# Kernel tuning notes

Measured on AMD Instinct MI355X. Metric: run time of the kernel, lower is better.

The kernel has to match this reference:

```python
import jax, jax.numpy as jnp
import numpy as np

B, E, H, S, V, K = 128, 512, 512, 2048, 83, 3
PAD = 82


def _pos_emb(n, e):
    pos = jnp.arange(n, dtype=jnp.float32)[:, None]                      # [n,1]
    k = jnp.exp(-jnp.log(10000.0) * jnp.arange(0, e, 2, dtype=jnp.float32) / e)  # [e/2]
    arg = pos * k                                                        # [n,e/2]
    pe = jnp.stack([jnp.sin(arg), jnp.cos(arg)], axis=-1).reshape(n, e)  # interleave sin/cos
    return pe.T                                                          # [e,n]


def setup_inputs() -> dict:
    key = jax.random.key(0)
    ks = jax.random.split(key, 8)
    return {
        "encoder_output": jax.random.normal(ks[0], (B, H, S), dtype=jnp.float32),
        "encoder_total": jax.random.normal(ks[1], (B, H, S), dtype=jnp.float32),
        "decoder_input": jax.random.randint(ks[2], (B,), 0, V),
        "count": 0,
        "emb": jax.random.normal(ks[3], (V, E), dtype=jnp.float32) * 0.02,
        "conv_w": jax.random.normal(ks[4], (2 * H, E, K), dtype=jnp.float32) * 0.02,
        "conv_b": jnp.zeros((2 * H,), dtype=jnp.float32),
        "lin2_w": jax.random.normal(ks[5], (V, H), dtype=jnp.float32) * 0.02,
        "lin2_b": jnp.zeros((V,), dtype=jnp.float32),
    }


def reference(encoder_output, encoder_total, decoder_input, count, emb, conv_w, conv_b, lin2_w, lin2_b):
    # count==0 first-step path; dropout is identity (inference).
    pe3 = _pos_emb(K, E)                                    # [E,K]

    def layer(dec_in):
        # dec_in: [B,E,K]
        xp = dec_in + pe3[None]                             # positional embedding add
        y = jnp.einsum('bek,oek->bo', xp, conv_w) + conv_b  # valid conv1d, out length 1 -> [B,2H]
        a, b = jnp.split(y, 2, axis=1)
        glu = a * jax.nn.sigmoid(b)                         # [B,H]
        d = glu + xp[:, :, -1]                              # residual with last (pe-added) column
        scores = jnp.einsum('bh,bhs->bs', d, encoder_output)
        attn = jax.nn.softmax(scores, axis=-1)              # [B,S]
        c = jnp.einsum('bs,bhs->bh', attn, encoder_total)   # [B,H]
        h = glu + c
        logits = h @ lin2_w.T + lin2_b                      # [B,V]
        return h, jax.nn.log_softmax(logits, axis=-1)

    x = emb[decoder_input][:, :, None]                      # [B,E,1]
    pad_col = jnp.broadcast_to(emb[PAD][None, :, None], (B, E, 1))
    dec1 = jnp.concatenate([pad_col, pad_col, x], axis=2)   # [B,E,3]

    h1, _ = layer(dec1)                                     # n_l = 0
    dec2 = jnp.concatenate([dec1[:, :, :2], h1[:, :, None]], axis=2)
    h2, _ = layer(dec2)                                     # n_l = 1
    dec3 = jnp.concatenate([dec1[:, :, :2], h2[:, :, None]], axis=2)
    h3, ls3 = layer(dec3)                                   # n_l = 2

    return (jax.nn.softmax(h3, axis=1)[:, :, None],         # [B,H,1]
            ls3[:, None, :])                                # [B,1,V]
```

## Files before the change

kernel.cpp:

```cpp
#include <hip/hip_runtime.h>
#include <math.h>

#define B_   128
#define E_   512
#define H_   512
#define S_   2048
#define V_   83
#define PAD_ 82

typedef float v4f __attribute__((ext_vector_type(4)));

__device__ __forceinline__ v4f ldnt4(const float* p) {
    return __builtin_nontemporal_load((const v4f*)p);
}


__global__ void k_misc(const float* __restrict__ emb, float* __restrict__ pe2,
                       float* __restrict__ x01i) {
    int e = threadIdx.x;
    float freq = expf(-9.210340371976184f * (float)(e & ~1) * (1.0f / 512.0f));
    float p0 = (e & 1) ? 1.0f : 0.0f;
    float p1 = (e & 1) ? cosf(freq) : sinf(freq);
    float p2 = (e & 1) ? cosf(2.0f * freq) : sinf(2.0f * freq);
    pe2[e] = p2;
    float ep = emb[PAD_ * 512 + e];
    x01i[e * 3 + 0] = ep + p0;
    x01i[e * 3 + 1] = ep + p1;
    x01i[e * 3 + 2] = 0.0f;
}

__global__ void k_base3(const float* __restrict__ cw, const float* __restrict__ x01i,
                        float* __restrict__ base) {
    int t = threadIdx.x, w = t >> 6, lane = t & 63;
    __shared__ float xs[1536];
    for (int j = t; j < 1536; j += 256) xs[j] = x01i[j];
    __syncthreads();
    int o = blockIdx.x * 4 + w;
    const float* rp = cw + (size_t)o * 1536 + lane * 4;
    float acc = 0.f;
    #pragma unroll
    for (int j = 0; j < 6; ++j) {
        float4 v = *(const float4*)(rp + j * 256);
        const float* xp = &xs[lane * 4 + j * 256];
        acc += v.x * xp[0] + v.y * xp[1] + v.z * xp[2] + v.w * xp[3];
    }
    #pragma unroll
    for (int off = 32; off > 0; off >>= 1) acc += __shfl_down(acc, off, 64);
    if (lane == 0) base[o] = acc;
}

__global__ void k_prep(const float* __restrict__ cw, float* __restrict__ W2t) {
    __shared__ float tile[64][129];
    int ob = blockIdx.x * 64, eb = blockIdx.y * 128;
    int t = threadIdx.x;
    for (int idx = t; idx < 8192; idx += 256) {
        int r = idx >> 7, e = idx & 127;
        tile[r][e] = cw[(size_t)(ob + r) * 1536 + (eb + e) * 3 + 2];
    }
    __syncthreads();
    for (int idx = t; idx < 8192; idx += 256) {
        int e = idx >> 6, o = idx & 63;
        W2t[(size_t)(eb + e) * 1024 + ob + o] = tile[o][e];
    }
}


__global__ void k_yx(int first, const int* __restrict__ tok, const float* __restrict__ emb,
                     const float* __restrict__ h, const float* __restrict__ pe2,
                     const float* __restrict__ W2t, const float* __restrict__ base,
                     const float* __restrict__ cb, float* __restrict__ xcol,
                     float* __restrict__ y) {
    int oc = blockIdx.x, bq = blockIdx.y, t = threadIdx.x;
    __shared__ float xs[4][512];
    for (int j = t; j < 2048; j += 256) {
        int bb = j >> 9, e = j & 511;
        int b = bq * 4 + bb;
        float v = first ? emb[tok[b] * 512 + e] : h[b * 512 + e];
        xs[bb][e] = v + pe2[e];
    }
    __syncthreads();
    if (oc == 0)
        for (int j = t; j < 2048; j += 256) xcol[bq * 2048 + j] = xs[j >> 9][j & 511];
    int o = oc * 256 + t;
    float init = base[o] + cb[o];
    float a0 = init, a1 = init, a2 = init, a3 = init;
    for (int e = 0; e < 512; ++e) {
        float w = W2t[e * 1024 + o];
        a0 += xs[0][e] * w; a1 += xs[1][e] * w;
        a2 += xs[2][e] * w; a3 += xs[3][e] * w;
    }
    int b0 = bq * 4;
    y[(size_t)(b0 + 0) * 1024 + o] = a0;
    y[(size_t)(b0 + 1) * 1024 + o] = a1;
    y[(size_t)(b0 + 2) * 1024 + o] = a2;
    y[(size_t)(b0 + 3) * 1024 + o] = a3;
}

__global__ void k_scores2(const float* __restrict__ y, const float* __restrict__ xcol,
                          const float* __restrict__ enc, float* __restrict__ part) {
    int hc = blockIdx.x, b = blockIdx.y, t = threadIdx.x;
    int w = t >> 6, lane = t & 63;
    __shared__ float dl[64];
    __shared__ float red[4 * 2048];
    if (t < 64) {
        int hg = hc * 64 + t;
        float ya = y[b * 1024 + hg];
        float yb_ = y[b * 1024 + 512 + hg];
        float g = ya / (1.0f + expf(-yb_));
        dl[t] = g + xcol[b * 512 + hg];
    }
    __syncthreads();
    v4f a[8];
    #pragma unroll
    for (int j = 0; j < 8; ++j) a[j] = (v4f)(0.f);
    const float* bp = enc + ((size_t)b * 512 + hc * 64 + w * 16) * 2048 + lane * 4;
    for (int r = 0; r < 16; ++r) {
        float dh = dl[w * 16 + r];
        const float* rp = bp + (size_t)r * 2048;
        #pragma unroll
        for (int j = 0; j < 8; ++j) {
            v4f v = ldnt4(rp + j * 256);
            a[j] += dh * v;
        }
    }
    #pragma unroll
    for (int j = 0; j < 8; ++j)
        *(v4f*)&red[w * 2048 + j * 256 + lane * 4] = a[j];
    __syncthreads();
    #pragma unroll
    for (int k = 0; k < 2; ++k) {
        int s = t * 4 + k * 1024;
        v4f s0 = *(const v4f*)&red[0 * 2048 + s];
        v4f s1 = *(const v4f*)&red[1 * 2048 + s];
        v4f s2 = *(const v4f*)&red[2 * 2048 + s];
        v4f s3 = *(const v4f*)&red[3 * 2048 + s];
        *(v4f*)&part[(size_t)hc * 262144 + b * 2048 + s] = (s0 + s1) + (s2 + s3);
    }
}

__global__ void k_softmax2(const float* __restrict__ part, float* __restrict__ attn) {
    int b = blockIdx.x, t = threadIdx.x;
    float v[8];
    float m = -1e30f;
    for (int i = 0; i < 8; ++i) {
        int s = i * 256 + t;
        float acc = 0.f;
        #pragma unroll
        for (int hc = 0; hc < 8; ++hc) acc += part[(size_t)hc * 262144 + b * 2048 + s];
        v[i] = acc; m = fmaxf(m, acc);
    }
    __shared__ float r[256];
    r[t] = m; __syncthreads();
    for (int s = 128; s > 0; s >>= 1) { if (t < s) r[t] = fmaxf(r[t], r[t + s]); __syncthreads(); }
    float M = r[0]; __syncthreads();
    float sum = 0.f;
    for (int i = 0; i < 8; ++i) { v[i] = expf(v[i] - M); sum += v[i]; }
    r[t] = sum; __syncthreads();
    for (int s = 128; s > 0; s >>= 1) { if (t < s) r[t] += r[t + s]; __syncthreads(); }
    float inv = 1.0f / r[0];
    for (int i = 0; i < 8; ++i) attn[b * 2048 + i * 256 + t] = v[i] * inv;
}

__global__ void k_c2(const float* __restrict__ attn, const float* __restrict__ enc,
                     const float* __restrict__ y, float* __restrict__ hbuf) {
    int t = threadIdx.x;
    int b  = blockIdx.x >> 7;
    int h0 = (blockIdx.x & 127) << 2;
    __shared__ float al[2048];
    for (int j = t; j < 2048; j += 256) al[j] = attn[b * 2048 + j];
    __syncthreads();
    int w = t >> 6, lane = t & 63;
    int hh = h0 + w;
    const float* vp = enc + ((size_t)b * 512 + hh) * 2048;
    float acc = 0.f;
    #pragma unroll
    for (int it = 0; it < 8; ++it) {
        int s = it * 256 + lane * 4;
        v4f v = ldnt4(vp + s);
        float4 p = *(const float4*)&al[s];
        acc += p.x * v[0] + p.y * v[1] + p.z * v[2] + p.w * v[3];
    }
    #pragma unroll
    for (int off = 32; off > 0; off >>= 1) acc += __shfl_down(acc, off, 64);
    if (lane == 0) {
        float ya = y[b * 1024 + hh];
        float yb_ = y[b * 1024 + 512 + hh];
        float g = ya / (1.0f + expf(-yb_));
        hbuf[b * 512 + hh] = g + acc;
    }
}


__global__ void k_epi(const float* __restrict__ h, const float* __restrict__ l2w,
                      const float* __restrict__ l2b, float* __restrict__ out) {
    int b = blockIdx.x, t = threadIdx.x;
    __shared__ float hl[512];
    hl[t] = h[b * 512 + t]; hl[t + 256] = h[b * 512 + 256 + t];
    __syncthreads();
    float acc = 0.f;
    if (t < V_) {
        acc = l2b[t];
        for (int e = 0; e < 512; ++e) acc += hl[e] * l2w[t * 512 + e];
    }
    __shared__ float r[256];
    r[t] = (t < V_) ? acc : -1e30f; __syncthreads();
    for (int s = 128; s > 0; s >>= 1) { if (t < s) r[t] = fmaxf(r[t], r[t + s]); __syncthreads(); }
    float M = r[0]; __syncthreads();
    r[t] = (t < V_) ? expf(acc - M) : 0.f; __syncthreads();
    for (int s = 128; s > 0; s >>= 1) { if (t < s) r[t] += r[t + s]; __syncthreads(); }
    float L = M + logf(r[0]);
    if (t < V_) out[65536 + b * V_ + t] = acc - L;
    __syncthreads();
    float v0 = hl[t], v1 = hl[t + 256];
    r[t] = fmaxf(v0, v1); __syncthreads();
    for (int s = 128; s > 0; s >>= 1) { if (t < s) r[t] = fmaxf(r[t], r[t + s]); __syncthreads(); }
    float M2 = r[0]; __syncthreads();
    float e0 = expf(v0 - M2), e1 = expf(v1 - M2);
    r[t] = e0 + e1; __syncthreads();
    for (int s = 128; s > 0; s >>= 1) { if (t < s) r[t] += r[t + s]; __syncthreads(); }
    float inv = 1.0f / r[0];
    out[b * 512 + t] = e0 * inv;
    out[b * 512 + 256 + t] = e1 * inv;
}


extern "C" void kernel_launch(void* const* d_in, const int* in_sizes, int n_in,
                              void* d_out, int out_size, void* d_ws, size_t ws_size,
                              hipStream_t stream) {
    const float* enc_out = (const float*)d_in[0];
    const float* enc_tot = (const float*)d_in[1];
    const int*   tok     = (const int*)d_in[2];
    const float* emb     = (const float*)d_in[4];
    const float* conv_w  = (const float*)d_in[5];
    const float* conv_b  = (const float*)d_in[6];
    const float* l2w     = (const float*)d_in[7];
    const float* l2b     = (const float*)d_in[8];
    float* out = (float*)d_out;
    float* ws = (float*)d_ws;

    float* W2t  = ws;
    float* base = W2t + 524288;
    float* pe2  = base + 1024;
    float* x01i = pe2 + 512;
    float* xcol = x01i + 1536;
    float* yb   = xcol + 65536;
    float* attn = yb + 131072;
    float* part = attn + 262144;
    float* hbuf = part + 2097152;

    k_misc<<<1, 512, 0, stream>>>(emb, pe2, x01i);
    k_base3<<<256, 256, 0, stream>>>(conv_w, x01i, base);
    k_prep<<<dim3(16, 4), 256, 0, stream>>>(conv_w, W2t);

    for (int L = 0; L < 3; ++L) {
        k_yx<<<dim3(4, 32), 256, 0, stream>>>(L == 0 ? 1 : 0, tok, emb, hbuf, pe2,
                                              W2t, base, conv_b, xcol, yb);
        k_scores2<<<dim3(8, 128), 256, 0, stream>>>(yb, xcol, enc_out, part);
        k_softmax2<<<128, 256, 0, stream>>>(part, attn);
        k_c2<<<16384, 256, 0, stream>>>(attn, enc_tot, yb, hbuf);
    }

    k_epi<<<128, 256, 0, stream>>>(hbuf, l2w, l2b, out);
}
```

Baseline: 630.2 us.

## Cache encoder_total as fp16 after first layer and retile yx, softmax, context kernels

On the first layer the context kernel reads encoder_total in fp32 and also writes an fp16 copy into the workspace. Layers two and three then read the half-size copy, which cuts HBM traffic for the bandwidth-bound attention-weighted sum. The rounding to fp16 is an accuracy risk and depends on the workspace being large enough. k_yx is rewritten to use 64 blocks with vectorized float4 weight loads over two batches each, softmax moves to 1024 threads, and the context kernel moves to 512-thread blocks.

```diff
diff --git a/kernel.cpp b/kernel.cpp
--- a/kernel.cpp
+++ b/kernel.cpp
@@ -9,6 +9,7 @@
 #define PAD_ 82
 
 typedef float v4f __attribute__((ext_vector_type(4)));
+typedef _Float16 h4 __attribute__((ext_vector_type(4)));
 
 __device__ __forceinline__ v4f ldnt4(const float* p) {
     return __builtin_nontemporal_load((const v4f*)p);
@@ -65,35 +66,35 @@
 }
 
 
-__global__ void k_yx(int first, const int* __restrict__ tok, const float* __restrict__ emb,
-                     const float* __restrict__ h, const float* __restrict__ pe2,
-                     const float* __restrict__ W2t, const float* __restrict__ base,
-                     const float* __restrict__ cb, float* __restrict__ xcol,
-                     float* __restrict__ y) {
-    int oc = blockIdx.x, bq = blockIdx.y, t = threadIdx.x;
-    __shared__ float xs[4][512];
-    for (int j = t; j < 2048; j += 256) {
+__global__ void k_yx2(int first, const int* __restrict__ tok, const float* __restrict__ emb,
+                      const float* __restrict__ h, const float* __restrict__ pe2,
+                      const float* __restrict__ W2t, const float* __restrict__ base,
+                      const float* __restrict__ cb, float* __restrict__ xcol,
+                      float* __restrict__ y) {
+    int bq = blockIdx.x, t = threadIdx.x;
+    __shared__ float xs[2][512];
+    for (int j = t; j < 1024; j += 256) {
         int bb = j >> 9, e = j & 511;
-        int b = bq * 4 + bb;
+        int b = bq * 2 + bb;
         float v = first ? emb[tok[b] * 512 + e] : h[b * 512 + e];
-        xs[bb][e] = v + pe2[e];
-    }
-    __syncthreads();
-    if (oc == 0)
-        for (int j = t; j < 2048; j += 256) xcol[bq * 2048 + j] = xs[j >> 9][j & 511];
-    int o = oc * 256 + t;
-    float init = base[o] + cb[o];
-    float a0 = init, a1 = init, a2 = init, a3 = init;
+        float x = v + pe2[e];
+        xs[bb][e] = x;
+        xcol[b * 512 + e] = x;
+    }
+    __syncthreads();
+    int o4 = t * 4;
+    v4f bs = *(const v4f*)&base[o4];
+    v4f cbs = *(const v4f*)&cb[o4];
+    v4f a0 = bs + cbs, a1 = a0;
+    #pragma unroll 4
     for (int e = 0; e < 512; ++e) {
-        float w = W2t[e * 1024 + o];
-        a0 += xs[0][e] * w; a1 += xs[1][e] * w;
-        a2 += xs[2][e] * w; a3 += xs[3][e] * w;
-    }
-    int b0 = bq * 4;
-    y[(size_t)(b0 + 0) * 1024 + o] = a0;
-    y[(size_t)(b0 + 1) * 1024 + o] = a1;
-    y[(size_t)(b0 + 2) * 1024 + o] = a2;
-    y[(size_t)(b0 + 3) * 1024 + o] = a3;
+        v4f w = *(const v4f*)&W2t[e * 1024 + o4];
+        a0 += xs[0][e] * w;
+        a1 += xs[1][e] * w;
+    }
+    int b0 = bq * 2;
+    *(v4f*)&y[(size_t)b0 * 1024 + o4] = a0;
+    *(v4f*)&y[(size_t)(b0 + 1) * 1024 + o4] = a1;
 }
 
 __global__ void k_scores2(const float* __restrict__ y, const float* __restrict__ xcol,
@@ -138,45 +139,54 @@
     }
 }
 
-__global__ void k_softmax2(const float* __restrict__ part, float* __restrict__ attn) {
+__global__ void k_softmax3(const float* __restrict__ part, float* __restrict__ attn) {
     int b = blockIdx.x, t = threadIdx.x;
-    float v[8];
-    float m = -1e30f;
-    for (int i = 0; i < 8; ++i) {
-        int s = i * 256 + t;
-        float acc = 0.f;
-        #pragma unroll
-        for (int hc = 0; hc < 8; ++hc) acc += part[(size_t)hc * 262144 + b * 2048 + s];
-        v[i] = acc; m = fmaxf(m, acc);
-    }
-    __shared__ float r[256];
-    r[t] = m; __syncthreads();
-    for (int s = 128; s > 0; s >>= 1) { if (t < s) r[t] = fmaxf(r[t], r[t + s]); __syncthreads(); }
+    float a0 = 0.f, a1 = 0.f;
+    #pragma unroll
+    for (int hc = 0; hc < 8; ++hc) {
+        const float* pp = part + (size_t)hc * 262144 + b * 2048;
+        a0 += pp[t]; a1 += pp[t + 1024];
+    }
+    __shared__ float r[1024];
+    r[t] = fmaxf(a0, a1); __syncthreads();
+    for (int s = 512; s > 0; s >>= 1) { if (t < s) r[t] = fmaxf(r[t], r[t + s]); __syncthreads(); }
     float M = r[0]; __syncthreads();
-    float sum = 0.f;
-    for (int i = 0; i < 8; ++i) { v[i] = expf(v[i] - M); sum += v[i]; }
-    r[t] = sum; __syncthreads();
-    for (int s = 128; s > 0; s >>= 1) { if (t < s) r[t] += r[t + s]; __syncthreads(); }
+    float e0 = expf(a0 - M), e1 = expf(a1 - M);
+    r[t] = e0 + e1; __syncthreads();
+    for (int s = 512; s > 0; s >>= 1) { if (t < s) r[t] += r[t + s]; __syncthreads(); }
     float inv = 1.0f / r[0];
-    for (int i = 0; i < 8; ++i) attn[b * 2048 + i * 256 + t] = v[i] * inv;
-}
-
-__global__ void k_c2(const float* __restrict__ attn, const float* __restrict__ enc,
-                     const float* __restrict__ y, float* __restrict__ hbuf) {
+    attn[b * 2048 + t] = e0 * inv;
+    attn[b * 2048 + t + 1024] = e1 * inv;
+}
+
+template <int MODE>
+__global__ void k_c3(const float* __restrict__ attn, const float* __restrict__ encf,
+                     _Float16* __restrict__ e16, const float* __restrict__ y,
+                     float* __restrict__ hbuf) {
     int t = threadIdx.x;
-    int b  = blockIdx.x >> 7;
-    int h0 = (blockIdx.x & 127) << 2;
+    int b  = blockIdx.x >> 6;
+    int h0 = (blockIdx.x & 63) << 3;
     __shared__ float al[2048];
-    for (int j = t; j < 2048; j += 256) al[j] = attn[b * 2048 + j];
+    for (int j = t; j < 2048; j += 512) al[j] = attn[b * 2048 + j];
     __syncthreads();
     int w = t >> 6, lane = t & 63;
     int hh = h0 + w;
-    const float* vp = enc + ((size_t)b * 512 + hh) * 2048;
+    size_t rowoff = ((size_t)b * 512 + hh) * 2048;
     float acc = 0.f;
     #pragma unroll
     for (int it = 0; it < 8; ++it) {
         int s = it * 256 + lane * 4;
-        v4f v = ldnt4(vp + s);
+        v4f v;
+        if (MODE == 2) {
+            h4 x = __builtin_nontemporal_load((const h4*)(e16 + rowoff + s));
+            v = (v4f){(float)x[0], (float)x[1], (float)x[2], (float)x[3]};
+        } else {
+            v = ldnt4(encf + rowoff + s);
+            if (MODE == 1) {
+                h4 x = {(_Float16)v[0], (_Float16)v[1], (_Float16)v[2], (_Float16)v[3]};
+                __builtin_nontemporal_store(x, (h4*)(e16 + rowoff + s));
+            }
+        }
         float4 p = *(const float4*)&al[s];
         acc += p.x * v[0] + p.y * v[1] + p.z * v[2] + p.w * v[3];
     }
@@ -247,17 +257,25 @@
     float* attn = yb + 131072;
     float* part = attn + 262144;
     float* hbuf = part + 2097152;
+    size_t nfloats = 3148800;
+    _Float16* e16 = (_Float16*)(ws + nfloats);
+    bool cache16 = ws_size >= nfloats * 4 + (size_t)134217728 * 2;
 
     k_misc<<<1, 512, 0, stream>>>(emb, pe2, x01i);
     k_base3<<<256, 256, 0, stream>>>(conv_w, x01i, base);
     k_prep<<<dim3(16, 4), 256, 0, stream>>>(conv_w, W2t);
 
     for (int L = 0; L < 3; ++L) {
-        k_yx<<<dim3(4, 32), 256, 0, stream>>>(L == 0 ? 1 : 0, tok, emb, hbuf, pe2,
-                                              W2t, base, conv_b, xcol, yb);
+        k_yx2<<<64, 256, 0, stream>>>(L == 0 ? 1 : 0, tok, emb, hbuf, pe2,
+                                      W2t, base, conv_b, xcol, yb);
         k_scores2<<<dim3(8, 128), 256, 0, stream>>>(yb, xcol, enc_out, part);
-        k_softmax2<<<128, 256, 0, stream>>>(part, attn);
-        k_c2<<<16384, 256, 0, stream>>>(attn, enc_tot, yb, hbuf);
+        k_softmax3<<<128, 1024, 0, stream>>>(part, attn);
+        if (!cache16)
+            k_c3<0><<<8192, 512, 0, stream>>>(attn, enc_tot, e16, yb, hbuf);
+        else if (L == 0)
+            k_c3<1><<<8192, 512, 0, stream>>>(attn, enc_tot, e16, yb, hbuf);
+        else
+            k_c3<2><<<8192, 512, 0, stream>>>(attn, enc_tot, e16, yb, hbuf);
     }
 
     k_epi<<<128, 256, 0, stream>>>(hbuf, l2w, l2b, out);
```

New measurement: 676.6 us. 7.4% more time.

## Fuse scores, softmax and context into split-S flash-style attention kernel

Applied to the files above, without the earlier changes.

Replaces the separate scores, softmax and context kernels with one kernel that splits S into four chunks per batch. Each block computes partial scores over all H, a local softmax (max and sum), and the partial context against encoder_total. A small combine kernel then merges the four chunks with online-softmax rescaling and applies the GLU residual. This removes the large partial-score buffer and the attention round trip through global memory. The cost is only 512 blocks for streaming about 1 GB of encoder data, plus a serial per-row shuffle reduction in the context phase, so bandwidth use may suffer.

```diff
diff --git a/kernel.cpp b/kernel.cpp
--- a/kernel.cpp
+++ b/kernel.cpp
@@ -96,98 +96,74 @@
     y[(size_t)(b0 + 3) * 1024 + o] = a3;
 }
 
-__global__ void k_scores2(const float* __restrict__ y, const float* __restrict__ xcol,
-                          const float* __restrict__ enc, float* __restrict__ part) {
-    int hc = blockIdx.x, b = blockIdx.y, t = threadIdx.x;
+__global__ void k_attn(const float* __restrict__ y, const float* __restrict__ xcol,
+                       const float* __restrict__ eo, const float* __restrict__ et,
+                       float* __restrict__ partC, float* __restrict__ partML) {
+    int sc = blockIdx.x, b = blockIdx.y, t = threadIdx.x;
     int w = t >> 6, lane = t & 63;
-    __shared__ float dl[64];
-    __shared__ float red[4 * 2048];
-    if (t < 64) {
-        int hg = hc * 64 + t;
-        float ya = y[b * 1024 + hg];
-        float yb_ = y[b * 1024 + 512 + hg];
+    __shared__ float dl[512];
+    __shared__ float red[4][512];
+    __shared__ float p[512];
+    __shared__ float r[256];
+    for (int j = t; j < 512; j += 256) {
+        float ya = y[b * 1024 + j], yb_ = y[b * 1024 + 512 + j];
         float g = ya / (1.0f + expf(-yb_));
-        dl[t] = g + xcol[b * 512 + hg];
-    }
-    __syncthreads();
-    v4f a[8];
-    #pragma unroll
-    for (int j = 0; j < 8; ++j) a[j] = (v4f)(0.f);
-    const float* bp = enc + ((size_t)b * 512 + hc * 64 + w * 16) * 2048 + lane * 4;
-    for (int r = 0; r < 16; ++r) {
-        float dh = dl[w * 16 + r];
-        const float* rp = bp + (size_t)r * 2048;
+        dl[j] = g + xcol[b * 512 + j];
+    }
+    __syncthreads();
+    v4f a0 = (v4f)(0.f), a1 = (v4f)(0.f);
+    const float* bp = eo + ((size_t)b * 512 + w * 128) * 2048 + sc * 512 + lane * 8;
+    for (int rr = 0; rr < 128; ++rr) {
+        float dh = dl[w * 128 + rr];
+        const float* rp = bp + (size_t)rr * 2048;
+        a0 += dh * ldnt4(rp);
+        a1 += dh * ldnt4(rp + 4);
+    }
+    *(v4f*)&red[w][lane * 8] = a0;
+    *(v4f*)&red[w][lane * 8 + 4] = a1;
+    __syncthreads();
+    float s0 = red[0][t] + red[1][t] + red[2][t] + red[3][t];
+    float s1 = red[0][t + 256] + red[1][t + 256] + red[2][t + 256] + red[3][t + 256];
+    r[t] = fmaxf(s0, s1); __syncthreads();
+    for (int st = 128; st > 0; st >>= 1) { if (t < st) r[t] = fmaxf(r[t], r[t + st]); __syncthreads(); }
+    float M = r[0]; __syncthreads();
+    float e0 = expf(s0 - M), e1 = expf(s1 - M);
+    p[t] = e0; p[t + 256] = e1;
+    r[t] = e0 + e1; __syncthreads();
+    for (int st = 128; st > 0; st >>= 1) { if (t < st) r[t] += r[t + st]; __syncthreads(); }
+    if (t == 0) { partML[(b * 4 + sc) * 2 + 0] = M; partML[(b * 4 + sc) * 2 + 1] = r[0]; }
+    __syncthreads();
+    const float* vp = et + ((size_t)b * 512 + w * 128) * 2048 + sc * 512 + lane * 8;
+    v4f pp0 = *(const v4f*)&p[lane * 8];
+    v4f pp1 = *(const v4f*)&p[lane * 8 + 4];
+    float* pc = partC + ((size_t)(b * 4 + sc)) * 512 + w * 128;
+    for (int rr = 0; rr < 128; ++rr) {
+        const float* rp = vp + (size_t)rr * 2048;
+        v4f m0 = pp0 * ldnt4(rp) + pp1 * ldnt4(rp + 4);
+        float acc = (m0[0] + m0[1]) + (m0[2] + m0[3]);
         #pragma unroll
-        for (int j = 0; j < 8; ++j) {
-            v4f v = ldnt4(rp + j * 256);
-            a[j] += dh * v;
-        }
-    }
-    #pragma unroll
-    for (int j = 0; j < 8; ++j)
-        *(v4f*)&red[w * 2048 + j * 256 + lane * 4] = a[j];
-    __syncthreads();
-    #pragma unroll
-    for (int k = 0; k < 2; ++k) {
-        int s = t * 4 + k * 1024;
-        v4f s0 = *(const v4f*)&red[0 * 2048 + s];
-        v4f s1 = *(const v4f*)&red[1 * 2048 + s];
-        v4f s2 = *(const v4f*)&red[2 * 2048 + s];
-        v4f s3 = *(const v4f*)&red[3 * 2048 + s];
-        *(v4f*)&part[(size_t)hc * 262144 + b * 2048 + s] = (s0 + s1) + (s2 + s3);
-    }
-}
-
-__global__ void k_softmax2(const float* __restrict__ part, float* __restrict__ attn) {
+        for (int off = 32; off > 0; off >>= 1) acc += __shfl_down(acc, off, 64);
+        if (lane == 0) pc[rr] = acc;
+    }
+}
+
+__global__ void k_comb(const float* __restrict__ partC, const float* __restrict__ partML,
+                       const float* __restrict__ y, float* __restrict__ hbuf) {
     int b = blockIdx.x, t = threadIdx.x;
-    float v[8];
-    float m = -1e30f;
-    for (int i = 0; i < 8; ++i) {
-        int s = i * 256 + t;
-        float acc = 0.f;
-        #pragma unroll
-        for (int hc = 0; hc < 8; ++hc) acc += part[(size_t)hc * 262144 + b * 2048 + s];
-        v[i] = acc; m = fmaxf(m, acc);
-    }
-    __shared__ float r[256];
-    r[t] = m; __syncthreads();
-    for (int s = 128; s > 0; s >>= 1) { if (t < s) r[t] = fmaxf(r[t], r[t + s]); __syncthreads(); }
-    float M = r[0]; __syncthreads();
-    float sum = 0.f;
-    for (int i = 0; i < 8; ++i) { v[i] = expf(v[i] - M); sum += v[i]; }
-    r[t] = sum; __syncthreads();
-    for (int s = 128; s > 0; s >>= 1) { if (t < s) r[t] += r[t + s]; __syncthreads(); }
-    float inv = 1.0f / r[0];
-    for (int i = 0; i < 8; ++i) attn[b * 2048 + i * 256 + t] = v[i] * inv;
-}
-
-__global__ void k_c2(const float* __restrict__ attn, const float* __restrict__ enc,
-                     const float* __restrict__ y, float* __restrict__ hbuf) {
-    int t = threadIdx.x;
-    int b  = blockIdx.x >> 7;
-    int h0 = (blockIdx.x & 127) << 2;
-    __shared__ float al[2048];
-    for (int j = t; j < 2048; j += 256) al[j] = attn[b * 2048 + j];
-    __syncthreads();
-    int w = t >> 6, lane = t & 63;
-    int hh = h0 + w;
-    const float* vp = enc + ((size_t)b * 512 + hh) * 2048;
-    float acc = 0.f;
-    #pragma unroll
-    for (int it = 0; it < 8; ++it) {
-        int s = it * 256 + lane * 4;
-        v4f v = ldnt4(vp + s);
-        float4 p = *(const float4*)&al[s];
-        acc += p.x * v[0] + p.y * v[1] + p.z * v[2] + p.w * v[3];
-    }
-    #pragma unroll
-    for (int off = 32; off > 0; off >>= 1) acc += __shfl_down(acc, off, 64);
-    if (lane == 0) {
-        float ya = y[b * 1024 + hh];
-        float yb_ = y[b * 1024 + 512 + hh];
-        float g = ya / (1.0f + expf(-yb_));
-        hbuf[b * 512 + hh] = g + acc;
-    }
+    float m0 = partML[(b * 4 + 0) * 2], l0 = partML[(b * 4 + 0) * 2 + 1];
+    float m1 = partML[(b * 4 + 1) * 2], l1 = partML[(b * 4 + 1) * 2 + 1];
+    float m2 = partML[(b * 4 + 2) * 2], l2 = partML[(b * 4 + 2) * 2 + 1];
+    float m3 = partML[(b * 4 + 3) * 2], l3 = partML[(b * 4 + 3) * 2 + 1];
+    float M = fmaxf(fmaxf(m0, m1), fmaxf(m2, m3));
+    float w0 = expf(m0 - M), w1 = expf(m1 - M), w2 = expf(m2 - M), w3 = expf(m3 - M);
+    float Z = w0 * l0 + w1 * l1 + w2 * l2 + w3 * l3;
+    float c = (w0 * partC[(size_t)(b * 4 + 0) * 512 + t] +
+               w1 * partC[(size_t)(b * 4 + 1) * 512 + t] +
+               w2 * partC[(size_t)(b * 4 + 2) * 512 + t] +
+               w3 * partC[(size_t)(b * 4 + 3) * 512 + t]) / Z;
+    float ya = y[b * 1024 + t], yb_ = y[b * 1024 + 512 + t];
+    float g = ya / (1.0f + expf(-yb_));
+    hbuf[b * 512 + t] = g + c;
 }
 
 
@@ -238,15 +214,15 @@
     float* out = (float*)d_out;
     float* ws = (float*)d_ws;
 
-    float* W2t  = ws;
-    float* base = W2t + 524288;
-    float* pe2  = base + 1024;
-    float* x01i = pe2 + 512;
-    float* xcol = x01i + 1536;
-    float* yb   = xcol + 65536;
-    float* attn = yb + 131072;
-    float* part = attn + 262144;
-    float* hbuf = part + 2097152;
+    float* W2t   = ws;
+    float* base  = W2t + 524288;
+    float* pe2   = base + 1024;
+    float* x01i  = pe2 + 512;
+    float* xcol  = x01i + 1536;
+    float* yb    = xcol + 65536;
+    float* hbuf  = yb + 131072;
+    float* partC = hbuf + 65536;
+    float* partML= partC + 262144;
 
     k_misc<<<1, 512, 0, stream>>>(emb, pe2, x01i);
     k_base3<<<256, 256, 0, stream>>>(conv_w, x01i, base);
@@ -255,9 +231,8 @@
     for (int L = 0; L < 3; ++L) {
         k_yx<<<dim3(4, 32), 256, 0, stream>>>(L == 0 ? 1 : 0, tok, emb, hbuf, pe2,
                                               W2t, base, conv_b, xcol, yb);
-        k_scores2<<<dim3(8, 128), 256, 0, stream>>>(yb, xcol, enc_out, part);
-        k_softmax2<<<128, 256, 0, stream>>>(part, attn);
-        k_c2<<<16384, 256, 0, stream>>>(attn, enc_tot, yb, hbuf);
+        k_attn<<<dim3(4, 128), 256, 0, stream>>>(yb, xcol, enc_out, enc_tot, partC, partML);
+        k_comb<<<128, 512, 0, stream>>>(partC, partML, yb, hbuf);
     }
 
     k_epi<<<128, 256, 0, stream>>>(hbuf, l2w, l2b, out);
```

New measurement: 819.4 us. 1.3x slower.

## Cache encoder_total as fp16 in workspace for layers two and three

Applied to the files above, without the earlier changes.

In the first layer the context kernel writes an fp16 copy of encoder_total into spare workspace while it computes. Layers two and three then read that half-size copy instead of the fp32 tensor, cutting the memory traffic of the bandwidth-bound context reduction. The cost is an extra write pass in layer one and reduced precision of the context vector in later layers. The path only applies to as many rows as the workspace can hold and falls back to fp32 otherwise.

```diff
diff --git a/kernel.cpp b/kernel.cpp
--- a/kernel.cpp
+++ b/kernel.cpp
@@ -9,6 +9,8 @@
 #define PAD_ 82
 
 typedef float v4f __attribute__((ext_vector_type(4)));
+typedef _Float16 h4 __attribute__((ext_vector_type(4)));
+typedef _Float16 h8 __attribute__((ext_vector_type(8)));
 
 __device__ __forceinline__ v4f ldnt4(const float* p) {
     return __builtin_nontemporal_load((const v4f*)p);
@@ -161,8 +163,10 @@
     for (int i = 0; i < 8; ++i) attn[b * 2048 + i * 256 + t] = v[i] * inv;
 }
 
-__global__ void k_c2(const float* __restrict__ attn, const float* __restrict__ enc,
-                     const float* __restrict__ y, float* __restrict__ hbuf) {
+template <int MODE>
+__global__ void k_c3(const float* __restrict__ attn, const float* __restrict__ encf,
+                     _Float16* __restrict__ e16, const float* __restrict__ y,
+                     float* __restrict__ hbuf, int R) {
     int t = threadIdx.x;
     int b  = blockIdx.x >> 7;
     int h0 = (blockIdx.x & 127) << 2;
@@ -171,14 +175,33 @@
     __syncthreads();
     int w = t >> 6, lane = t & 63;
     int hh = h0 + w;
-    const float* vp = enc + ((size_t)b * 512 + hh) * 2048;
+    int row = b * 512 + hh;
+    size_t rowoff = (size_t)row * 2048;
     float acc = 0.f;
-    #pragma unroll
-    for (int it = 0; it < 8; ++it) {
-        int s = it * 256 + lane * 4;
-        v4f v = ldnt4(vp + s);
-        float4 p = *(const float4*)&al[s];
-        acc += p.x * v[0] + p.y * v[1] + p.z * v[2] + p.w * v[3];
+    if (MODE == 2 && row < R) {
+        #pragma unroll
+        for (int it = 0; it < 4; ++it) {
+            int s = it * 512 + lane * 8;
+            h8 x = __builtin_nontemporal_load((const h8*)(e16 + rowoff + s));
+            float4 p0 = *(const float4*)&al[s];
+            float4 p1 = *(const float4*)&al[s + 4];
+            acc += p0.x * (float)x[0] + p0.y * (float)x[1]
+                 + p0.z * (float)x[2] + p0.w * (float)x[3]
+                 + p1.x * (float)x[4] + p1.y * (float)x[5]
+                 + p1.z * (float)x[6] + p1.w * (float)x[7];
+        }
+    } else {
+        #pragma unroll
+        for (int it = 0; it < 8; ++it) {
+            int s = it * 256 + lane * 4;
+            v4f v = ldnt4(encf + rowoff + s);
+            if (MODE == 1 && row < R) {
+                h4 x = {(_Float16)v[0], (_Float16)v[1], (_Float16)v[2], (_Float16)v[3]};
+                __builtin_nontemporal_store(x, (h4*)(e16 + rowoff + s));
+            }
+            float4 p = *(const float4*)&al[s];
+            acc += p.x * v[0] + p.y * v[1] + p.z * v[2] + p.w * v[3];
+        }
     }
     #pragma unroll
     for (int off = 32; off > 0; off >>= 1) acc += __shfl_down(acc, off, 64);
@@ -247,6 +270,15 @@
     float* attn = yb + 131072;
     float* part = attn + 262144;
     float* hbuf = part + 2097152;
+    size_t nfloats = 3148800;
+    _Float16* e16 = (_Float16*)(ws + nfloats);
+
+    int R = 0;
+    size_t base_bytes = nfloats * 4;
+    if (ws_size > base_bytes) {
+        size_t rows = (ws_size - base_bytes) / 4096;
+        R = (int)(rows > 65536 ? 65536 : rows);
+    }
 
     k_misc<<<1, 512, 0, stream>>>(emb, pe2, x01i);
     k_base3<<<256, 256, 0, stream>>>(conv_w, x01i, base);
@@ -257,7 +289,12 @@
                                               W2t, base, conv_b, xcol, yb);
         k_scores2<<<dim3(8, 128), 256, 0, stream>>>(yb, xcol, enc_out, part);
         k_softmax2<<<128, 256, 0, stream>>>(part, attn);
-        k_c2<<<16384, 256, 0, stream>>>(attn, enc_tot, yb, hbuf);
+        if (R == 0)
+            k_c3<0><<<16384, 256, 0, stream>>>(attn, enc_tot, e16, yb, hbuf, R);
+        else if (L == 0)
+            k_c3<1><<<16384, 256, 0, stream>>>(attn, enc_tot, e16, yb, hbuf, R);
+        else
+            k_c3<2><<<16384, 256, 0, stream>>>(attn, enc_tot, e16, yb, hbuf, R);
     }
 
     k_epi<<<128, 256, 0, stream>>>(hbuf, l2w, l2b, out);
```

Measured after the change: 631.7 us. Within noise of the previous version (+0.2%).
